# Optimization experiments

Measured on AMD Instinct MI355X. Metric: run time of the kernel, lower is better.

The kernel has to match this reference:

```python
import jax, jax.numpy as jnp
import numpy as np

B, E, F, H, C = 2048, 16, 512, 1024, 512
TOP_K = 4
TEMP = 1.0


def setup_inputs() -> dict:
    key = jax.random.key(0)
    ks = jax.random.split(key, 5)
    h = jax.random.normal(ks[0], (B, F), jnp.float32)
    # Router posterior params (xavier-ish mu, logvar init at -7 as in torch code)
    W_mu = jax.random.normal(ks[1], (E, F), jnp.float32) * (1.0 / np.sqrt(F))
    W_logvar = jnp.full((E, F), -7.0, jnp.float32)
    b_mu = jnp.zeros((E,), jnp.float32)
    b_logvar = jnp.full((E,), -7.0, jnp.float32)
    # Expert MLP params: layer1 [F->H] relu, layer2 [H->C]
    W1 = jax.random.normal(ks[2], (E, F, H), jnp.float32) * (1.0 / np.sqrt(F))
    b1 = jnp.zeros((E, H), jnp.float32)
    W2 = jax.random.normal(ks[3], (E, H, C), jnp.float32) * (1.0 / np.sqrt(H))
    b2 = jnp.zeros((E, C), jnp.float32)
    return {"h": h, "W_mu": W_mu, "b_mu": b_mu, "W_logvar": W_logvar,
            "b_logvar": b_logvar, "W1": W1, "b1": b1, "W2": W2, "b2": b2}


def reference(h, W_mu, b_mu, W_logvar, b_logvar, W1, b1, W2, b2):
    # Bayesian router moments: mu = h @ W_mu^T + b_mu ; var = (h*h) @ exp(W_logvar)^T + exp(b_logvar)
    mu_m = h @ W_mu.T + b_mu                                   # [B,E]
    var_m = (h * h) @ jnp.exp(W_logvar).T + jnp.exp(b_logvar)  # [B,E]
    var_m = jnp.maximum(var_m, 1e-12)
    # Logistic-normal shrink: tilde = mu / sqrt(1 + (pi/8) var)
    tilde_m = mu_m / jnp.sqrt(1.0 + (jnp.pi / 8.0) * var_m)
    gate_probs = jax.nn.softmax(tilde_m / TEMP, axis=-1)       # [B,E]
    # Strict top-k by gate_scores (tilde_m), renormalize probs within top-k
    topk_scores, topk_idx = jax.lax.top_k(tilde_m, TOP_K)      # [B,k]
    topk_w = jnp.take_along_axis(gate_probs, topk_idx, axis=1) # [B,k]
    topk_w = topk_w / jnp.maximum(topk_w.sum(axis=1, keepdims=True), 1e-12)
    # Dense combine weights: w[b,e] = sum of renormalized top-k weights of token b for expert e
    Bsz = h.shape[0]
    w = jnp.zeros((Bsz, E), h.dtype).at[jnp.arange(Bsz)[:, None], topk_idx].add(topk_w)
    # Expert MLPs (grouped GEMM form); tokens not routed to expert e get weight 0
    a = jax.nn.relu(jnp.einsum('bf,efh->beh', h, W1) + b1)     # [B,E,H]
    y = jnp.einsum('beh,ehc->bec', a, W2) + b2                 # [B,E,C]
    combined = jnp.einsum('be,bec->bc', w, y)                  # [B,C]
    return combined
```

## Files before the change

kernel.cpp:

```cpp
#include <hip/hip_runtime.h>
#include <hip/hip_bf16.h>

typedef __attribute__((ext_vector_type(8))) short bf16x8;
typedef __attribute__((ext_vector_type(4))) float f32x4;

#define NTOK   2048
#define NEXP   16
#define NF     512
#define NH     1024
#define NCOUT  512
#define NPAIR  8192

__device__ __forceinline__ void gload16_lds(const __hip_bfloat16* g, const __hip_bfloat16* l) {
  __builtin_amdgcn_global_load_lds((const __attribute__((address_space(1))) void*)g,
                                   (__attribute__((address_space(3))) void*)l, 16, 0, 0);
}

__global__ __launch_bounds__(256) void precompute_kernel(
    const float* __restrict__ W_logvar, const float* __restrict__ b_logvar,
    float* __restrict__ expW, float* __restrict__ expb)
{
  int i = blockIdx.x * 256 + threadIdx.x;
  if (i < NEXP * NF) expW[i] = expf(W_logvar[i]);
  if (i < NEXP) expb[i] = expf(b_logvar[i]);
}

__global__ __launch_bounds__(256) void router_kernel(
    const float* __restrict__ h, const float* __restrict__ W_mu,
    const float* __restrict__ b_mu, const float* __restrict__ expW,
    const float* __restrict__ expb,
    int* __restrict__ topk_idx, float* __restrict__ topk_w,
    __hip_bfloat16* __restrict__ hb)
{
  __shared__ __align__(16) float hs[NF], hs2[NF];
  __shared__ float smu[NEXP], svar[NEXP];
  const int b = blockIdx.x, tid = threadIdx.x;
  for (int i = tid; i < NF; i += 256) {
    float v = h[(size_t)b * NF + i];
    hs[i] = v; hs2[i] = v * v;
    hb[(size_t)b * NF + i] = __float2bfloat16(v);
  }
  __syncthreads();
  const int e = tid >> 4, l = tid & 15;
  float mu = 0.f, var = 0.f;
  const float4* wm4 = (const float4*)(W_mu + e * NF);
  const float4* wv4 = (const float4*)(expW + e * NF);
  const float4* h4  = (const float4*)hs;
  const float4* h24 = (const float4*)hs2;
#pragma unroll
  for (int j = 0; j < NF / 64; ++j) {
    int i4 = l + j * 16;
    float4 a = h4[i4],  wa = wm4[i4];
    float4 c = h24[i4], wc = wv4[i4];
    mu  += a.x * wa.x + a.y * wa.y + a.z * wa.z + a.w * wa.w;
    var += c.x * wc.x + c.y * wc.y + c.z * wc.z + c.w * wc.w;
  }
#pragma unroll
  for (int o = 1; o < 16; o <<= 1) { mu += __shfl_xor(mu, o); var += __shfl_xor(var, o); }
  if (l == 0) { smu[e] = mu + b_mu[e]; svar[e] = var + expb[e]; }
  __syncthreads();
  if (tid < 64) {
    float val = -1e30f;
    if (tid < NEXP) {
      float v = fmaxf(svar[tid], 1e-12f);
      val = smu[tid] / sqrtf(1.0f + 0.39269908169872414f * v);
    }
    float mx = 0.f, wsum = 0.f;
    int i0, i1, i2, i3; float p0, p1, p2, p3;
#define TOPK_ROUND(ii, pp, FIRST)                                          \
    {                                                                      \
      float m = val;                                                       \
      m = fmaxf(m, __shfl_xor(m, 1));  m = fmaxf(m, __shfl_xor(m, 2));     \
      m = fmaxf(m, __shfl_xor(m, 4));  m = fmaxf(m, __shfl_xor(m, 8));     \
      m = fmaxf(m, __shfl_xor(m, 16)); m = fmaxf(m, __shfl_xor(m, 32));    \
      unsigned long long bm = __ballot(val == m);                          \
      int bi = (int)__builtin_ctzll(bm);                                   \
      if (FIRST) mx = m;                                                   \
      pp = expf(m - mx); wsum += pp; ii = bi;                              \
      if (tid == bi) val = -1e30f;                                         \
    }
    TOPK_ROUND(i0, p0, 1)
    TOPK_ROUND(i1, p1, 0)
    TOPK_ROUND(i2, p2, 0)
    TOPK_ROUND(i3, p3, 0)
#undef TOPK_ROUND
    if (tid == 0) {
      float inv = 1.0f / fmaxf(wsum, 1e-12f);
      topk_idx[b * 4 + 0] = i0; topk_w[b * 4 + 0] = p0 * inv;
      topk_idx[b * 4 + 1] = i1; topk_w[b * 4 + 1] = p1 * inv;
      topk_idx[b * 4 + 2] = i2; topk_w[b * 4 + 2] = p2 * inv;
      topk_idx[b * 4 + 3] = i3; topk_w[b * 4 + 3] = p3 * inv;
    }
  }
}

__global__ __launch_bounds__(256) void count_kernel(
    const int* __restrict__ topk_idx, int* __restrict__ counts)
{
  const int e = blockIdx.x;
  int c = 0;
  for (int i = threadIdx.x; i < NPAIR; i += 256) c += (topk_idx[i] == e);
#pragma unroll
  for (int o = 1; o < 64; o <<= 1) c += __shfl_xor(c, o);
  __shared__ int ws[4];
  if ((threadIdx.x & 63) == 0) ws[threadIdx.x >> 6] = c;
  __syncthreads();
  if (threadIdx.x == 0) counts[e] = ws[0] + ws[1] + ws[2] + ws[3];
}

__global__ void offsets_kernel(const int* __restrict__ counts, int* __restrict__ offsets) {
  if (threadIdx.x == 0) {
    int run = 0;
    for (int e = 0; e < NEXP; ++e) { offsets[e] = run; run += counts[e]; }
  }
}

__global__ __launch_bounds__(256) void scatter_kernel(
    const int* __restrict__ topk_idx,
    const int* __restrict__ offsets,
    int* __restrict__ token_of_row, int* __restrict__ pair_row)
{
  const int e = blockIdx.x;
  __shared__ int wsum[4];
  __shared__ int chunk_base;
  if (threadIdx.x == 0) chunk_base = offsets[e];
  __syncthreads();
  const int wid = threadIdx.x >> 6, lane = threadIdx.x & 63;
  for (int c0 = 0; c0 < NPAIR; c0 += 256) {
    const int t = c0 + threadIdx.x;
    const bool f = (topk_idx[t] == e);
    const unsigned long long m = __ballot(f);
    const int pre = __popcll(m & ((1ull << lane) - 1ull));
    if (lane == 0) wsum[wid] = __popcll(m);
    __syncthreads();
    int wbase = 0;
#pragma unroll
    for (int i = 0; i < 4; ++i) if (i < wid) wbase += wsum[i];
    const int total = wsum[0] + wsum[1] + wsum[2] + wsum[3];
    if (f) {
      const int pos = chunk_base + wbase + pre;
      token_of_row[pos] = t >> 2;
      pair_row[t] = pos;
    }
    __syncthreads();
    if (threadIdx.x == 0) chunk_base += total;
  }
}

__global__ __launch_bounds__(256) void transpose_convert_kernel(
    const float* __restrict__ in, __hip_bfloat16* __restrict__ out, int R, int C)
{
  __shared__ float tile[32][33];
  const int e = blockIdx.z;
  const int r0 = blockIdx.y * 32, c0 = blockIdx.x * 32;
  const int x = threadIdx.x & 31, y = threadIdx.x >> 5;
  const float* ip = in + ((size_t)e * R + r0) * C + c0;
#pragma unroll
  for (int i = 0; i < 4; ++i) tile[y + 8 * i][x] = ip[(size_t)(y + 8 * i) * C + x];
  __syncthreads();
  __hip_bfloat16* op = out + ((size_t)e * C + c0) * R + r0;
#pragma unroll
  for (int i = 0; i < 4; ++i) op[(size_t)(y + 8 * i) * R + x] = __float2bfloat16(tile[x][y + 8 * i]);
}


__global__ __launch_bounds__(256) void gemm1_kernel(
    const __hip_bfloat16* __restrict__ hb,
    const __hip_bfloat16* __restrict__ W1t,
    const float* __restrict__ b1,
    const int* __restrict__ token_of_row, const int* __restrict__ offsets,
    const int* __restrict__ counts,
    __hip_bfloat16* __restrict__ a_out)
{
  const int bid = blockIdx.x;
  const int id  = (bid & 7) * 512 + (bid >> 3);
  const int e   = id >> 8;
  const int m0  = ((id >> 4) & 15) * 128;
  const int n0  = (id & 15) * 64;
  const int cnt = counts[e];
  if (m0 >= cnt) return;
  const int off = offsets[e];

  __shared__ __align__(16) __hip_bfloat16 As[128 * 64];
  __shared__ __align__(16) __hip_bfloat16 Bs[64 * 64];

  const int tid = threadIdx.x;
  const int w = tid >> 6, l = tid & 63;
  const int wm = w >> 1, wn = w & 1;
  const int r16 = l & 15, g4 = l >> 4;
  const int sx = r16 & 7;
  const int koffL = (((l & 7) ^ (l >> 3)) * 8);

  const __hip_bfloat16* Aptr[4];
#pragma unroll
  for (int i = 0; i < 4; ++i) {
    int r = off + m0 + w * 32 + i * 8 + (l >> 3);
    if (r > NPAIR - 1) r = NPAIR - 1;
    Aptr[i] = hb + (size_t)token_of_row[r] * NF + koffL;
  }
  const __hip_bfloat16* Bptr[2];
#pragma unroll
  for (int i = 0; i < 2; ++i)
    Bptr[i] = W1t + ((size_t)e * NH + n0 + w * 16 + i * 8 + (l >> 3)) * NF + koffL;

  f32x4 acc[4][2] = {};

  for (int k0 = 0; k0 < NF; k0 += 64) {
    __syncthreads();
#pragma unroll
    for (int i = 0; i < 4; ++i) gload16_lds(Aptr[i] + k0, As + (w * 32 + i * 8) * 64);
#pragma unroll
    for (int i = 0; i < 2; ++i) gload16_lds(Bptr[i] + k0, Bs + (w * 16 + i * 8) * 64);
    __syncthreads();
#pragma unroll
    for (int ks = 0; ks < 2; ++ks) {
      const int seg = (ks * 4 + g4) ^ sx;
      bf16x8 af[4], bq[2];
#pragma unroll
      for (int rr = 0; rr < 4; ++rr)
        af[rr] = *(const bf16x8*)(As + (wm * 64 + rr * 16 + r16) * 64 + seg * 8);
#pragma unroll
      for (int nn = 0; nn < 2; ++nn)
        bq[nn] = *(const bf16x8*)(Bs + (wn * 32 + nn * 16 + r16) * 64 + seg * 8);
#pragma unroll
      for (int rr = 0; rr < 4; ++rr)
#pragma unroll
        for (int nn = 0; nn < 2; ++nn)
          acc[rr][nn] = __builtin_amdgcn_mfma_f32_16x16x32_bf16(af[rr], bq[nn], acc[rr][nn], 0, 0, 0);
    }
  }

  const int q4 = l >> 4, cl = l & 15;
  const int mmax = cnt - m0;
#pragma unroll
  for (int rr = 0; rr < 4; ++rr) {
#pragma unroll
    for (int nn = 0; nn < 2; ++nn) {
      const int c = n0 + wn * 32 + nn * 16 + cl;
      const float bias = b1[e * NH + c];
#pragma unroll
      for (int q = 0; q < 4; ++q) {
        const int r = wm * 64 + rr * 16 + q4 * 4 + q;
        if (r < mmax) {
          float v = fmaxf(acc[rr][nn][q] + bias, 0.f);
          a_out[(size_t)(off + m0 + r) * NH + c] = __float2bfloat16(v);
        }
      }
    }
  }
}

__global__ __launch_bounds__(256) void gemm2_kernel(
    const __hip_bfloat16* __restrict__ a_in,
    const __hip_bfloat16* __restrict__ W2t,
    const float* __restrict__ b2,
    const int* __restrict__ offsets, const int* __restrict__ counts,
    float* __restrict__ ybuf)
{
  const int bid = blockIdx.x;
  const int id  = (bid & 7) * 256 + (bid >> 3);
  const int e   = id >> 7;
  const int m0  = ((id >> 3) & 15) * 128;
  const int n0  = (id & 7) * 64;
  const int cnt = counts[e];
  if (m0 >= cnt) return;
  const int off = offsets[e];

  __shared__ __align__(16) __hip_bfloat16 As[128 * 64];
  __shared__ __align__(16) __hip_bfloat16 Bs[64 * 64];

  const int tid = threadIdx.x;
  const int w = tid >> 6, l = tid & 63;
  const int wm = w >> 1, wn = w & 1;
  const int r16 = l & 15, g4 = l >> 4;
  const int sx = r16 & 7;
  const int koffL = (((l & 7) ^ (l >> 3)) * 8);

  const __hip_bfloat16* Aptr[4];
#pragma unroll
  for (int i = 0; i < 4; ++i) {
    int r = off + m0 + w * 32 + i * 8 + (l >> 3);
    if (r > NPAIR - 1) r = NPAIR - 1;
    Aptr[i] = a_in + (size_t)r * NH + koffL;
  }
  const __hip_bfloat16* Bptr[2];
#pragma unroll
  for (int i = 0; i < 2; ++i)
    Bptr[i] = W2t + ((size_t)e * NCOUT + n0 + w * 16 + i * 8 + (l >> 3)) * NH + koffL;

  f32x4 acc[4][2] = {};

  for (int k0 = 0; k0 < NH; k0 += 64) {
    __syncthreads();
#pragma unroll
    for (int i = 0; i < 4; ++i) gload16_lds(Aptr[i] + k0, As + (w * 32 + i * 8) * 64);
#pragma unroll
    for (int i = 0; i < 2; ++i) gload16_lds(Bptr[i] + k0, Bs + (w * 16 + i * 8) * 64);
    __syncthreads();
#pragma unroll
    for (int ks = 0; ks < 2; ++ks) {
      const int seg = (ks * 4 + g4) ^ sx;
      bf16x8 af[4], bq[2];
#pragma unroll
      for (int rr = 0; rr < 4; ++rr)
        af[rr] = *(const bf16x8*)(As + (wm * 64 + rr * 16 + r16) * 64 + seg * 8);
#pragma unroll
      for (int nn = 0; nn < 2; ++nn)
        bq[nn] = *(const bf16x8*)(Bs + (wn * 32 + nn * 16 + r16) * 64 + seg * 8);
#pragma unroll
      for (int rr = 0; rr < 4; ++rr)
#pragma unroll
        for (int nn = 0; nn < 2; ++nn)
          acc[rr][nn] = __builtin_amdgcn_mfma_f32_16x16x32_bf16(af[rr], bq[nn], acc[rr][nn], 0, 0, 0);
    }
  }

  const int q4 = l >> 4, cl = l & 15;
  const int mmax = cnt - m0;
#pragma unroll
  for (int rr = 0; rr < 4; ++rr) {
#pragma unroll
    for (int nn = 0; nn < 2; ++nn) {
      const int c = n0 + wn * 32 + nn * 16 + cl;
      const float bias = b2[e * NCOUT + c];
#pragma unroll
      for (int q = 0; q < 4; ++q) {
        const int r = wm * 64 + rr * 16 + q4 * 4 + q;
        if (r < mmax)
          ybuf[(size_t)(off + m0 + r) * NCOUT + c] = acc[rr][nn][q] + bias;
      }
    }
  }
}

__global__ __launch_bounds__(256) void combine_kernel(
    const float* __restrict__ ybuf, const int* __restrict__ pair_row,
    const float* __restrict__ topk_w, float* __restrict__ out)
{
  const int tok = blockIdx.x;
  const int c = threadIdx.x * 2;
  float a0 = 0.f, a1 = 0.f;
#pragma unroll
  for (int k = 0; k < 4; ++k) {
    const int t = tok * 4 + k;
    const float wt = topk_w[t];
    const float2 y = *(const float2*)(ybuf + (size_t)pair_row[t] * NCOUT + c);
    a0 += wt * y.x; a1 += wt * y.y;
  }
  *(float2*)(out + (size_t)tok * NCOUT + c) = make_float2(a0, a1);
}

extern "C" void kernel_launch(void* const* d_in, const int* in_sizes, int n_in,
                              void* d_out, int out_size, void* d_ws, size_t ws_size,
                              hipStream_t stream) {
  (void)in_sizes; (void)n_in; (void)ws_size; (void)out_size;
  const float* h        = (const float*)d_in[0];
  const float* W_mu     = (const float*)d_in[1];
  const float* b_mu     = (const float*)d_in[2];
  const float* W_logvar = (const float*)d_in[3];
  const float* b_logvar = (const float*)d_in[4];
  const float* W1       = (const float*)d_in[5];
  const float* b1       = (const float*)d_in[6];
  const float* W2       = (const float*)d_in[7];
  const float* b2       = (const float*)d_in[8];
  float* out = (float*)d_out;

  char* p = (char*)d_ws;
  int*   counts   = (int*)p;   p += 16 * 4;
  int*   offsets  = (int*)p;   p += 16 * 4;
  float* expb     = (float*)p; p += 16 * 4;
  p += 16 * 4;
  float* expW     = (float*)p; p += (size_t)NEXP * NF * 4;
  int*   topk_idx = (int*)p;   p += (size_t)NPAIR * 4;
  float* topk_w   = (float*)p; p += (size_t)NPAIR * 4;
  int*   tok_row  = (int*)p;   p += (size_t)NPAIR * 4;
  int*   pair_row = (int*)p;   p += (size_t)NPAIR * 4;
  __hip_bfloat16* hb   = (__hip_bfloat16*)p; p += (size_t)NTOK * NF * 2;
  __hip_bfloat16* W1t  = (__hip_bfloat16*)p; p += (size_t)NEXP * NF * NH * 2;
  __hip_bfloat16* W2t  = (__hip_bfloat16*)p; p += (size_t)NEXP * NH * NCOUT * 2;
  __hip_bfloat16* abuf = (__hip_bfloat16*)p; p += (size_t)NPAIR * NH * 2;
  float*          ybuf = (float*)p;          p += (size_t)NPAIR * NCOUT * 4;

  precompute_kernel<<<(NEXP * NF + 255) / 256, 256, 0, stream>>>(W_logvar, b_logvar, expW, expb);
  router_kernel<<<NTOK, 256, 0, stream>>>(h, W_mu, b_mu, expW, expb, topk_idx, topk_w, hb);
  count_kernel<<<NEXP, 256, 0, stream>>>(topk_idx, counts);
  offsets_kernel<<<1, 64, 0, stream>>>(counts, offsets);
  scatter_kernel<<<NEXP, 256, 0, stream>>>(topk_idx, offsets, tok_row, pair_row);

  transpose_convert_kernel<<<dim3(NH / 32, NF / 32, NEXP), 256, 0, stream>>>(W1, W1t, NF, NH);
  transpose_convert_kernel<<<dim3(NCOUT / 32, NH / 32, NEXP), 256, 0, stream>>>(W2, W2t, NH, NCOUT);

  gemm1_kernel<<<4096, 256, 0, stream>>>(hb, W1t, b1, tok_row, offsets, counts, abuf);
  gemm2_kernel<<<2048, 256, 0, stream>>>(abuf, W2t, b2, offsets, counts, ybuf);
  combine_kernel<<<NTOK, 256, 0, stream>>>(ybuf, pair_row, topk_w, out);
}
```

Measured before the change: 100.1 us.

## Merge routing kernels, widen transpose stores, double-buffer GEMM LDS tiles

Three separate routing kernels (count, offsets, scatter) become one 1024-thread block that computes per-chunk per-expert counts with ballots, prefix sums and scatters in a single pass, removing two launches and the sequential per-expert scans. The weight transpose/convert kernel now handles 64-row tiles and writes packed pairs of bf16 values as 32-bit stores. Both grouped GEMMs switch to double-buffered LDS so the next K-tile's global-to-LDS load is issued before computing on the current one, removing one barrier per iteration. This doubles LDS use per block and may reduce occupancy.

```diff
diff --git a/kernel.cpp b/kernel.cpp
--- a/kernel.cpp
+++ b/kernel.cpp
@@ -94,73 +94,77 @@
   }
 }
 
-__global__ __launch_bounds__(256) void count_kernel(
-    const int* __restrict__ topk_idx, int* __restrict__ counts)
-{
-  const int e = blockIdx.x;
-  int c = 0;
-  for (int i = threadIdx.x; i < NPAIR; i += 256) c += (topk_idx[i] == e);
-#pragma unroll
-  for (int o = 1; o < 64; o <<= 1) c += __shfl_xor(c, o);
-  __shared__ int ws[4];
-  if ((threadIdx.x & 63) == 0) ws[threadIdx.x >> 6] = c;
-  __syncthreads();
-  if (threadIdx.x == 0) counts[e] = ws[0] + ws[1] + ws[2] + ws[3];
-}
-
-__global__ void offsets_kernel(const int* __restrict__ counts, int* __restrict__ offsets) {
-  if (threadIdx.x == 0) {
+__global__ __launch_bounds__(1024) void route_finish_kernel(
+    const int* __restrict__ topk_idx,
+    int* __restrict__ counts, int* __restrict__ offsets,
+    int* __restrict__ token_of_row, int* __restrict__ pair_row)
+{
+  __shared__ int cnt[128][16];
+  __shared__ int choff[128][16];
+  __shared__ int tot[16];
+  __shared__ int soff[16];
+  const int tid = threadIdx.x;
+  const int wv = tid >> 6, ln = tid & 63;
+  int mye[8], myrank[8];
+#pragma unroll
+  for (int r = 0; r < 8; ++r) {
+    const int chunk = r * 16 + wv;
+    const int t = chunk * 64 + ln;
+    const int e = topk_idx[t];
+    mye[r] = e;
+    unsigned long long mymask = 0;
+#pragma unroll
+    for (int ee = 0; ee < 16; ++ee) {
+      unsigned long long b = __ballot(e == ee);
+      if (ln == 0) cnt[chunk][ee] = __popcll(b);
+      if (e == ee) mymask = b;
+    }
+    myrank[r] = __popcll(mymask & ((1ull << ln) - 1ull));
+  }
+  __syncthreads();
+  if (tid < 16) {
     int run = 0;
-    for (int e = 0; e < NEXP; ++e) { offsets[e] = run; run += counts[e]; }
-  }
-}
-
-__global__ __launch_bounds__(256) void scatter_kernel(
-    const int* __restrict__ topk_idx,
-    const int* __restrict__ offsets,
-    int* __restrict__ token_of_row, int* __restrict__ pair_row)
-{
-  const int e = blockIdx.x;
-  __shared__ int wsum[4];
-  __shared__ int chunk_base;
-  if (threadIdx.x == 0) chunk_base = offsets[e];
-  __syncthreads();
-  const int wid = threadIdx.x >> 6, lane = threadIdx.x & 63;
-  for (int c0 = 0; c0 < NPAIR; c0 += 256) {
-    const int t = c0 + threadIdx.x;
-    const bool f = (topk_idx[t] == e);
-    const unsigned long long m = __ballot(f);
-    const int pre = __popcll(m & ((1ull << lane) - 1ull));
-    if (lane == 0) wsum[wid] = __popcll(m);
-    __syncthreads();
-    int wbase = 0;
-#pragma unroll
-    for (int i = 0; i < 4; ++i) if (i < wid) wbase += wsum[i];
-    const int total = wsum[0] + wsum[1] + wsum[2] + wsum[3];
-    if (f) {
-      const int pos = chunk_base + wbase + pre;
-      token_of_row[pos] = t >> 2;
-      pair_row[t] = pos;
-    }
-    __syncthreads();
-    if (threadIdx.x == 0) chunk_base += total;
+    for (int c = 0; c < 128; ++c) { choff[c][tid] = run; run += cnt[c][tid]; }
+    tot[tid] = run;
+    counts[tid] = run;
+  }
+  __syncthreads();
+  if (tid == 0) {
+    int run = 0;
+    for (int e2 = 0; e2 < NEXP; ++e2) { soff[e2] = run; offsets[e2] = run; run += tot[e2]; }
+  }
+  __syncthreads();
+#pragma unroll
+  for (int r = 0; r < 8; ++r) {
+    const int chunk = r * 16 + wv;
+    const int t = chunk * 64 + ln;
+    const int e = mye[r];
+    const int pos = soff[e] + choff[chunk][e] + myrank[r];
+    token_of_row[pos] = t >> 2;
+    pair_row[t] = pos;
   }
 }
 
 __global__ __launch_bounds__(256) void transpose_convert_kernel(
     const float* __restrict__ in, __hip_bfloat16* __restrict__ out, int R, int C)
 {
-  __shared__ float tile[32][33];
+  __shared__ float tile[64][33];
   const int e = blockIdx.z;
-  const int r0 = blockIdx.y * 32, c0 = blockIdx.x * 32;
+  const int r0 = blockIdx.y * 64, c0 = blockIdx.x * 32;
   const int x = threadIdx.x & 31, y = threadIdx.x >> 5;
   const float* ip = in + ((size_t)e * R + r0) * C + c0;
 #pragma unroll
-  for (int i = 0; i < 4; ++i) tile[y + 8 * i][x] = ip[(size_t)(y + 8 * i) * C + x];
-  __syncthreads();
-  __hip_bfloat16* op = out + ((size_t)e * C + c0) * R + r0;
-#pragma unroll
-  for (int i = 0; i < 4; ++i) op[(size_t)(y + 8 * i) * R + x] = __float2bfloat16(tile[x][y + 8 * i]);
+  for (int i = 0; i < 8; ++i) tile[y + 8 * i][x] = ip[(size_t)(y + 8 * i) * C + x];
+  __syncthreads();
+  const int rp = threadIdx.x & 31, cb = threadIdx.x >> 5;
+#pragma unroll
+  for (int j = 0; j < 4; ++j) {
+    const int c = cb + 8 * j;
+    union { __hip_bfloat16 b[2]; unsigned u; } v;
+    v.b[0] = __float2bfloat16(tile[2 * rp][c]);
+    v.b[1] = __float2bfloat16(tile[2 * rp + 1][c]);
+    *(unsigned*)(out + ((size_t)e * C + c0 + c) * R + r0 + 2 * rp) = v.u;
+  }
 }
 
 
@@ -181,8 +185,8 @@
   if (m0 >= cnt) return;
   const int off = offsets[e];
 
-  __shared__ __align__(16) __hip_bfloat16 As[128 * 64];
-  __shared__ __align__(16) __hip_bfloat16 Bs[64 * 64];
+  __shared__ __align__(16) __hip_bfloat16 As[2][128 * 64];
+  __shared__ __align__(16) __hip_bfloat16 Bs[2][64 * 64];
 
   const int tid = threadIdx.x;
   const int w = tid >> 6, l = tid & 63;
@@ -203,25 +207,28 @@
   for (int i = 0; i < 2; ++i)
     Bptr[i] = W1t + ((size_t)e * NH + n0 + w * 16 + i * 8 + (l >> 3)) * NF + koffL;
 
+#define STG1(b, k0) { \
+  _Pragma("unroll") for (int i = 0; i < 4; ++i) gload16_lds(Aptr[i] + (k0), &As[b][(w * 32 + i * 8) * 64]); \
+  _Pragma("unroll") for (int i = 0; i < 2; ++i) gload16_lds(Bptr[i] + (k0), &Bs[b][(w * 16 + i * 8) * 64]); }
+
   f32x4 acc[4][2] = {};
-
-  for (int k0 = 0; k0 < NF; k0 += 64) {
+  const int NT = NF / 64;
+
+  STG1(0, 0)
+  for (int t = 0; t < NT; ++t) {
     __syncthreads();
-#pragma unroll
-    for (int i = 0; i < 4; ++i) gload16_lds(Aptr[i] + k0, As + (w * 32 + i * 8) * 64);
-#pragma unroll
-    for (int i = 0; i < 2; ++i) gload16_lds(Bptr[i] + k0, Bs + (w * 16 + i * 8) * 64);
-    __syncthreads();
+    const int cur = t & 1;
+    if (t + 1 < NT) STG1(cur ^ 1, (t + 1) * 64)
 #pragma unroll
     for (int ks = 0; ks < 2; ++ks) {
       const int seg = (ks * 4 + g4) ^ sx;
       bf16x8 af[4], bq[2];
 #pragma unroll
       for (int rr = 0; rr < 4; ++rr)
-        af[rr] = *(const bf16x8*)(As + (wm * 64 + rr * 16 + r16) * 64 + seg * 8);
+        af[rr] = *(const bf16x8*)(&As[cur][(wm * 64 + rr * 16 + r16) * 64 + seg * 8]);
 #pragma unroll
       for (int nn = 0; nn < 2; ++nn)
-        bq[nn] = *(const bf16x8*)(Bs + (wn * 32 + nn * 16 + r16) * 64 + seg * 8);
+        bq[nn] = *(const bf16x8*)(&Bs[cur][(wn * 32 + nn * 16 + r16) * 64 + seg * 8]);
 #pragma unroll
       for (int rr = 0; rr < 4; ++rr)
 #pragma unroll
@@ -229,6 +236,7 @@
           acc[rr][nn] = __builtin_amdgcn_mfma_f32_16x16x32_bf16(af[rr], bq[nn], acc[rr][nn], 0, 0, 0);
     }
   }
+#undef STG1
 
   const int q4 = l >> 4, cl = l & 15;
   const int mmax = cnt - m0;
@@ -266,8 +274,8 @@
   if (m0 >= cnt) return;
   const int off = offsets[e];
 
-  __shared__ __align__(16) __hip_bfloat16 As[128 * 64];
-  __shared__ __align__(16) __hip_bfloat16 Bs[64 * 64];
+  __shared__ __align__(16) __hip_bfloat16 As[2][128 * 64];
+  __shared__ __align__(16) __hip_bfloat16 Bs[2][64 * 64];
 
   const int tid = threadIdx.x;
   const int w = tid >> 6, l = tid & 63;
@@ -288,25 +296,28 @@
   for (int i = 0; i < 2; ++i)
     Bptr[i] = W2t + ((size_t)e * NCOUT + n0 + w * 16 + i * 8 + (l >> 3)) * NH + koffL;
 
+#define STG2(b, k0) { \
+  _Pragma("unroll") for (int i = 0; i < 4; ++i) gload16_lds(Aptr[i] + (k0), &As[b][(w * 32 + i * 8) * 64]); \
+  _Pragma("unroll") for (int i = 0; i < 2; ++i) gload16_lds(Bptr[i] + (k0), &Bs[b][(w * 16 + i * 8) * 64]); }
+
   f32x4 acc[4][2] = {};
-
-  for (int k0 = 0; k0 < NH; k0 += 64) {
+  const int NT = NH / 64;
+
+  STG2(0, 0)
+  for (int t = 0; t < NT; ++t) {
     __syncthreads();
-#pragma unroll
-    for (int i = 0; i < 4; ++i) gload16_lds(Aptr[i] + k0, As + (w * 32 + i * 8) * 64);
-#pragma unroll
-    for (int i = 0; i < 2; ++i) gload16_lds(Bptr[i] + k0, Bs + (w * 16 + i * 8) * 64);
-    __syncthreads();
+    const int cur = t & 1;
+    if (t + 1 < NT) STG2(cur ^ 1, (t + 1) * 64)
 #pragma unroll
     for (int ks = 0; ks < 2; ++ks) {
       const int seg = (ks * 4 + g4) ^ sx;
       bf16x8 af[4], bq[2];
 #pragma unroll
       for (int rr = 0; rr < 4; ++rr)
-        af[rr] = *(const bf16x8*)(As + (wm * 64 + rr * 16 + r16) * 64 + seg * 8);
+        af[rr] = *(const bf16x8*)(&As[cur][(wm * 64 + rr * 16 + r16) * 64 + seg * 8]);
 #pragma unroll
       for (int nn = 0; nn < 2; ++nn)
-        bq[nn] = *(const bf16x8*)(Bs + (wn * 32 + nn * 16 + r16) * 64 + seg * 8);
+        bq[nn] = *(const bf16x8*)(&Bs[cur][(wn * 32 + nn * 16 + r16) * 64 + seg * 8]);
 #pragma unroll
       for (int rr = 0; rr < 4; ++rr)
 #pragma unroll
@@ -314,6 +325,7 @@
           acc[rr][nn] = __builtin_amdgcn_mfma_f32_16x16x32_bf16(af[rr], bq[nn], acc[rr][nn], 0, 0, 0);
     }
   }
+#undef STG2
 
   const int q4 = l >> 4, cl = l & 15;
   const int mmax = cnt - m0;
@@ -383,12 +395,10 @@
 
   precompute_kernel<<<(NEXP * NF + 255) / 256, 256, 0, stream>>>(W_logvar, b_logvar, expW, expb);
   router_kernel<<<NTOK, 256, 0, stream>>>(h, W_mu, b_mu, expW, expb, topk_idx, topk_w, hb);
-  count_kernel<<<NEXP, 256, 0, stream>>>(topk_idx, counts);
-  offsets_kernel<<<1, 64, 0, stream>>>(counts, offsets);
-  scatter_kernel<<<NEXP, 256, 0, stream>>>(topk_idx, offsets, tok_row, pair_row);
-
-  transpose_convert_kernel<<<dim3(NH / 32, NF / 32, NEXP), 256, 0, stream>>>(W1, W1t, NF, NH);
-  transpose_convert_kernel<<<dim3(NCOUT / 32, NH / 32, NEXP), 256, 0, stream>>>(W2, W2t, NH, NCOUT);
+  route_finish_kernel<<<1, 1024, 0, stream>>>(topk_idx, counts, offsets, tok_row, pair_row);
+
+  transpose_convert_kernel<<<dim3(NH / 32, NF / 64, NEXP), 256, 0, stream>>>(W1, W1t, NF, NH);
+  transpose_convert_kernel<<<dim3(NCOUT / 32, NH / 64, NEXP), 256, 0, stream>>>(W2, W2t, NH, NCOUT);
 
   gemm1_kernel<<<4096, 256, 0, stream>>>(hb, W1t, b1, tok_row, offsets, counts, abuf);
   gemm2_kernel<<<2048, 256, 0, stream>>>(abuf, W2t, b2, offsets, counts, ybuf);
```

Measured after the change: 102.6 us. 2.5% more time.
